# Performance work log

Measured on AMD Instinct MI355X. Metric: run time of the kernel, lower is better.

## Reference

```python
import jax, jax.numpy as jnp
import numpy as np
import math

BS, H, L, D = 4, 8, 1024, 64
P = 513  # max_path_num + 1


def setup_inputs() -> dict:
    key = jax.random.key(0)
    ks = jax.random.split(key, 6)
    return {
        "query": jax.random.normal(ks[0], (BS, H, L, D), dtype=jnp.float32),
        "key": jax.random.normal(ks[1], (BS, H, L, D), dtype=jnp.float32),
        "value": jax.random.normal(ks[2], (BS, H, L, D), dtype=jnp.float32),
        "relation": jax.random.normal(ks[3], (BS, P, D), dtype=jnp.float32),
        "path_map": jax.random.randint(ks[4], (BS, L, L), 0, P, dtype=jnp.int32),
        "mask": jax.random.randint(ks[5], (BS, 1, L, L), 0, 2, dtype=jnp.int32),
    }


def reference(query, key, value, relation, path_map, mask):
    bs, h, Lc, d = query.shape
    p = relation.shape[1]
    # content score: bs,h,L,L
    score = jnp.einsum("bhik,bhjk->bhij", query, key)
    # relation score. Torch gathers with index of shape (bs,1,L,L) from a
    # (bs,h,L,P) tensor, which reads head 0 only and broadcasts over heads.
    score_r_h0 = jnp.einsum("bik,bpk->bip", query[:, 0], relation)  # bs,L,P
    gathered = jnp.take_along_axis(score_r_h0, path_map, axis=-1)   # bs,L,L
    score = score + gathered[:, None, :, :]
    scores = score / math.sqrt(d)
    scores = jnp.where(mask == 0, jnp.float32(-1e9), scores)
    p_attn = jax.nn.softmax(scores, axis=-1)  # bs,h,L,L
    attn_sum = jnp.einsum("bhij,bhjk->bhik", p_attn, value)
    # scatter-add attention probs into relation buckets: bs,h,L,P
    b_ix = jnp.arange(bs)[:, None, None, None]
    h_ix = jnp.arange(h)[None, :, None, None]
    i_ix = jnp.arange(Lc)[None, None, :, None]
    pm = jnp.broadcast_to(path_map[:, None, :, :], (bs, h, Lc, Lc))
    r_buckets = jnp.zeros((bs, h, Lc, p), dtype=p_attn.dtype).at[b_ix, h_ix, i_ix, pm].add(p_attn)
    r_attn_sum = jnp.einsum("bhip,bpk->bhik", r_buckets, relation)
    attn_sum = attn_sum + r_attn_sum
    return (attn_sum, p_attn)
```

## Files before the change

kernel.cpp:

```cpp
#include <hip/hip_runtime.h>


#define BSZ 4
#define NH 8
#define LSEQ 1024
#define DH 64
#define NP 513
#define TI 16
#define NT 1024
#define SRX 548
#define RTC 544

#define NQE (BSZ*NH*LSEQ*DH)
#define NRT (BSZ*DH*RTC)
#define NSR (BSZ*LSEQ*NP)
#define NGPW (2*BSZ*LSEQ*LSEQ)
#define OFF_QH 0
#define OFF_QL (NQE)
#define OFF_KH (2*NQE)
#define OFF_KL (3*NQE)
#define OFF_VT (4*NQE)
#define OFF_RT (5*NQE)
#define OFF_SR (5*NQE + NRT)
#define OFF_GP (5*NQE + NRT + NSR)
#define WS_NEED ((size_t)(OFF_GP + NGPW) * 2)

#define NB_QK 4096
#define NB_VT 512
#define NB_RT 544
#define NB_SR 256
#define NB_P1 (NB_QK + NB_VT + NB_RT + NB_SR)

typedef __attribute__((ext_vector_type(8))) short bf16x8;
typedef __attribute__((ext_vector_type(4))) float f32x4;
typedef __attribute__((ext_vector_type(4))) ushort u16x4;
typedef __attribute__((ext_vector_type(4))) uint u32x4;

__device__ __forceinline__ ushort f2bf(float x) {
    uint u = __float_as_uint(x);
    u += 0x7FFFu + ((u >> 16) & 1u);
    return (ushort)(u >> 16);
}
__device__ __forceinline__ float bf2f(ushort h) {
    return __uint_as_float(((uint)h) << 16);
}


__global__ __launch_bounds__(256) void prep1(
    const float* __restrict__ Q, const float* __restrict__ K,
    const float* __restrict__ V, const float* __restrict__ REL,
    ushort* __restrict__ ws)
{
    __shared__ float sT[64 * 65];
    const int bid = blockIdx.x;
    const int tid = threadIdx.x;

    if (bid < NB_QK) {
        const int n4 = NQE / 4;
        int i = bid * 256 + tid;
        int isK = i >= n4;
        int base = i - isK * n4;
        float4 v = ((const float4*)(isK ? K : Q))[base];
        float xs[4] = {v.x, v.y, v.z, v.w};
        u16x4 hh, ll;
        #pragma unroll
        for (int e = 0; e < 4; ++e) {
            ushort hi = f2bf(xs[e]);
            hh[e] = hi;
            ll[e] = f2bf(xs[e] - bf2f(hi));
        }
        *(u16x4*)(ws + (isK ? OFF_KH : OFF_QH) + (size_t)base * 4) = hh;
        *(u16x4*)(ws + (isK ? OFF_KL : OFF_QL) + (size_t)base * 4) = ll;
    } else if (bid < NB_QK + NB_VT) {
        const int vb = bid - NB_QK;
        const int bh = vb >> 4;
        const int j0 = (vb & 15) * 64;
        const float* Vb = V + ((size_t)bh << 16);
        for (int i = tid; i < 1024; i += 256) {
            int jr = i >> 4, c4 = i & 15;
            float4 vv = *(const float4*)(Vb + (size_t)(j0 + jr) * DH + c4 * 4);
            float* dst = &sT[jr * 65 + c4 * 4];
            dst[0] = vv.x; dst[1] = vv.y; dst[2] = vv.z; dst[3] = vv.w;
        }
        __syncthreads();
        const int d = tid >> 2, jseg = tid & 3;
        ushort* dst = ws + OFF_VT + ((size_t)bh << 16) + (size_t)d * LSEQ + j0 + jseg * 16;
        #pragma unroll
        for (int g = 0; g < 4; ++g) {
            u16x4 o;
            #pragma unroll
            for (int e = 0; e < 4; ++e)
                o[e] = f2bf(sT[(jseg * 16 + g * 4 + e) * 65 + d]);
            *(u16x4*)(dst + g * 4) = o;
        }
    } else if (bid < NB_QK + NB_VT + NB_RT) {
        int i = (bid - NB_QK - NB_VT) * 256 + tid;
        int b = i / (DH * RTC);
        int r = i - b * (DH * RTC);
        int d = r / RTC;
        int p = r - d * RTC;
        float x = (p < NP) ? REL[((size_t)b * NP + p) * DH + d] : 0.f;
        ws[OFF_RT + i] = f2bf(x);
    } else {
        const int sb = bid - (NB_QK + NB_VT + NB_RT);
        const int it = sb & 63, b = sb >> 6;
        const int i0 = it * TI;
        const int w = tid >> 6, l = tid & 63, lg = l >> 4, lm = l & 15;

        const float* Qb0 = Q + ((size_t)b * NH) * LSEQ * DH;
        const float* RELb = REL + (size_t)b * NP * DH;
        ushort* SRb = ws + OFF_SR + (size_t)b * LSEQ * NP;

        bf16x8 qh[2], ql[2];
        #pragma unroll
        for (int ks = 0; ks < 2; ++ks) {
            const float* qs = Qb0 + (size_t)(i0 + lm) * DH + ks * 32 + lg * 8;
            float4 v0 = *(const float4*)(qs);
            float4 v1 = *(const float4*)(qs + 4);
            float xs[8] = {v0.x, v0.y, v0.z, v0.w, v1.x, v1.y, v1.z, v1.w};
            #pragma unroll
            for (int e = 0; e < 8; ++e) {
                ushort hi = f2bf(xs[e]);
                qh[ks][e] = (short)hi;
                ql[ks][e] = (short)f2bf(xs[e] - bf2f(hi));
            }
        }

        for (int ct = w; ct < 33; ct += 4) {
            int p0 = ct * 16;
            int prow = p0 + lm; if (prow > 512) prow = 512;
            f32x4 a0 = {0.f, 0.f, 0.f, 0.f};
            #pragma unroll
            for (int ks = 0; ks < 2; ++ks) {
                const float* bsrc = RELb + (size_t)prow * DH + ks * 32 + lg * 8;
                float4 v0 = *(const float4*)(bsrc);
                float4 v1 = *(const float4*)(bsrc + 4);
                float xs[8] = {v0.x, v0.y, v0.z, v0.w, v1.x, v1.y, v1.z, v1.w};
                bf16x8 bh8, bl8;
                #pragma unroll
                for (int e = 0; e < 8; ++e) {
                    ushort hi = f2bf(xs[e]);
                    bh8[e] = (short)hi;
                    bl8[e] = (short)f2bf(xs[e] - bf2f(hi));
                }
                a0 = __builtin_amdgcn_mfma_f32_16x16x32_bf16(qh[ks], bh8, a0, 0, 0, 0);
                a0 = __builtin_amdgcn_mfma_f32_16x16x32_bf16(ql[ks], bh8, a0, 0, 0, 0);
                a0 = __builtin_amdgcn_mfma_f32_16x16x32_bf16(qh[ks], bl8, a0, 0, 0, 0);
            }
            if (p0 + lm < NP) {
                #pragma unroll
                for (int e = 0; e < 4; ++e)
                    SRb[(size_t)(i0 + 4 * lg + e) * NP + p0 + lm] = f2bf(a0[e]);
            }
        }
    }
}


__global__ __launch_bounds__(256) void prep2(
    const int* __restrict__ PM, const int* __restrict__ MASK,
    ushort* __restrict__ ws)
{
    __shared__ ushort sSR[4 * 520];
    const int tid = threadIdx.x;
    const int bid = blockIdx.x;
    const int b = bid >> 8;
    const int row0 = (bid & 255) * 4;

    const ushort* SRb = ws + OFF_SR + (size_t)b * LSEQ * NP;
    uint* GPb = (uint*)(ws + OFF_GP) + (size_t)b * LSEQ * LSEQ;
    const int* PMb = PM + (size_t)b * LSEQ * LSEQ;
    const int* MKb = MASK + (size_t)b * LSEQ * LSEQ;

    for (int i = tid; i < 4 * 520; i += 256) {
        int row = i / 520, col = i - row * 520;
        if (col < NP) sSR[row * 520 + col] = SRb[(size_t)(row0 + row) * NP + col];
    }
    __syncthreads();

    #pragma unroll
    for (int r = 0; r < 4; ++r) {
        int idx4 = r * 256 + tid;
        int row = idx4 >> 8;
        int c0 = (idx4 & 255) * 4;
        size_t off = (size_t)(row0 + row) * LSEQ + c0;
        int4 pm4 = *(const int4*)(PMb + off);
        int4 mk4 = *(const int4*)(MKb + off);
        const ushort* srow = &sSR[row * 520];
        u32x4 o;
        o[0] = ((uint)(mk4.x ? srow[pm4.x] : 0xFF62u) << 16) | (uint)pm4.x;
        o[1] = ((uint)(mk4.y ? srow[pm4.y] : 0xFF62u) << 16) | (uint)pm4.y;
        o[2] = ((uint)(mk4.z ? srow[pm4.z] : 0xFF62u) << 16) | (uint)pm4.z;
        o[3] = ((uint)(mk4.w ? srow[pm4.w] : 0xFF62u) << 16) | (uint)pm4.w;
        *(u32x4*)(GPb + off) = o;
    }
}


__global__ __launch_bounds__(NT, 4) void raa_main(
    const ushort* __restrict__ ws,
    float* __restrict__ OUT_A, float* __restrict__ OUT_P)
{
    __shared__ float  X[TI * SRX];
    __shared__ ushort sPb[TI * 1024];
    __shared__ float  sAttn[TI * DH];
    __shared__ float  sRedM[16 * 17];
    __shared__ float  sRedS[16 * 17];

    const int tid = threadIdx.x;
    const int w  = tid >> 6;
    const int l  = tid & 63;
    const int lg = l >> 4;
    const int lm = l & 15;

    const int it = blockIdx.x, h = blockIdx.y, b = blockIdx.z;
    const int i0 = it * TI;
    const int bh = b * NH + h;

    const ushort* Qh = ws + OFF_QH + (size_t)bh * LSEQ * DH;
    const ushort* Ql = ws + OFF_QL + (size_t)bh * LSEQ * DH;
    const ushort* Kh = ws + OFF_KH + (size_t)bh * LSEQ * DH;
    const ushort* Kl = ws + OFF_KL + (size_t)bh * LSEQ * DH;
    const ushort* Vt = ws + OFF_VT + (size_t)bh * DH * LSEQ;
    const ushort* Rt = ws + OFF_RT + (size_t)b * DH * RTC;
    const uint*   GPb = (const uint*)(ws + OFF_GP) + (size_t)b * LSEQ * LSEQ;

    #pragma unroll
    for (int z = 0; z < 9; ++z) {
        int idx = z * NT + tid;
        if (idx < TI * SRX) X[idx] = 0.f;
    }
    sAttn[tid] = 0.f;

    uint gp[16];
    #pragma unroll
    for (int t = 0; t < 4; ++t) {
        #pragma unroll
        for (int e = 0; e < 4; ++e) {
            int col = (4 * w + t) * 16 + lm;
            int row = 4 * lg + e;
            gp[t * 4 + e] = GPb[(size_t)(i0 + row) * LSEQ + col];
        }
    }

    bf16x8 qhh[2], qhl[2];
    #pragma unroll
    for (int ks = 0; ks < 2; ++ks) {
        size_t ao = (size_t)(i0 + lm) * DH + ks * 32 + lg * 8;
        qhh[ks] = *(const bf16x8*)(Qh + ao);
        qhl[ks] = *(const bf16x8*)(Ql + ao);
    }

    f32x4 acc[4];
    bf16x8 kh_c[2], kl_c[2], kh_n[2], kl_n[2];
    {
        size_t bo = (size_t)(4 * w * 16 + lm) * DH + lg * 8;
        kh_c[0] = *(const bf16x8*)(Kh + bo);      kl_c[0] = *(const bf16x8*)(Kl + bo);
        kh_c[1] = *(const bf16x8*)(Kh + bo + 32); kl_c[1] = *(const bf16x8*)(Kl + bo + 32);
    }
    #pragma unroll
    for (int t = 0; t < 4; ++t) {
        if (t < 3) {
            size_t bo = (size_t)((4 * w + t + 1) * 16 + lm) * DH + lg * 8;
            kh_n[0] = *(const bf16x8*)(Kh + bo);      kl_n[0] = *(const bf16x8*)(Kl + bo);
            kh_n[1] = *(const bf16x8*)(Kh + bo + 32); kl_n[1] = *(const bf16x8*)(Kl + bo + 32);
        }
        acc[t] = (f32x4){0.f, 0.f, 0.f, 0.f};
        #pragma unroll
        for (int ks = 0; ks < 2; ++ks) {
            acc[t] = __builtin_amdgcn_mfma_f32_16x16x32_bf16(qhh[ks], kh_c[ks], acc[t], 0, 0, 0);
            acc[t] = __builtin_amdgcn_mfma_f32_16x16x32_bf16(qhl[ks], kh_c[ks], acc[t], 0, 0, 0);
            acc[t] = __builtin_amdgcn_mfma_f32_16x16x32_bf16(qhh[ks], kl_c[ks], acc[t], 0, 0, 0);
        }
        #pragma unroll
        for (int ks = 0; ks < 2; ++ks) {
            kh_c[ks] = kh_n[ks]; kl_c[ks] = kl_n[ks];
        }
    }

    #pragma unroll
    for (int i = 0; i < 16; ++i) {
        int t = i >> 2, e = i & 3;
        float g = bf2f((ushort)(gp[i] >> 16));
        acc[t][e] = (g < -1e30f) ? -1e9f : (acc[t][e] + g) * 0.125f;
    }

    float mw[4], c4v[4];
    #pragma unroll
    for (int e = 0; e < 4; ++e) {
        float m = fmaxf(fmaxf(acc[0][e], acc[1][e]), fmaxf(acc[2][e], acc[3][e]));
        #pragma unroll
        for (int o = 8; o >= 1; o >>= 1) m = fmaxf(m, __shfl_xor(m, o));
        mw[e] = m;
        float s = 0.f;
        #pragma unroll
        for (int t = 0; t < 4; ++t) {
            float v = __expf(acc[t][e] - m);
            acc[t][e] = v;
            s += v;
        }
        #pragma unroll
        for (int o = 8; o >= 1; o >>= 1) s += __shfl_xor(s, o);
        if (lm == 0) {
            sRedM[(4 * lg + e) * 17 + w] = m;
            sRedS[(4 * lg + e) * 17 + w] = s;
        }
    }
    __syncthreads();
    #pragma unroll
    for (int e = 0; e < 4; ++e) {
        int row = 4 * lg + e;
        float mv = sRedM[row * 17 + lm];
        float sv = sRedS[row * 17 + lm];
        float m = mv;
        #pragma unroll
        for (int o = 8; o >= 1; o >>= 1) m = fmaxf(m, __shfl_xor(m, o));
        float sp = sv * __expf(mv - m);
        #pragma unroll
        for (int o = 8; o >= 1; o >>= 1) sp += __shfl_xor(sp, o);
        c4v[e] = __expf(mw[e] - m) / sp;
    }

    #pragma unroll
    for (int t = 0; t < 4; ++t) {
        int col = (4 * w + t) * 16 + lm;
        #pragma unroll
        for (int e = 0; e < 4; ++e) {
            int row = 4 * lg + e;
            float p = acc[t][e] * c4v[e];
            sPb[row * 1024 + (((col >> 3) ^ (row & 7)) << 3) + (col & 7)] = f2bf(p);
            atomicAdd(&X[row * SRX + (int)(gp[t * 4 + e] & 0xFFFFu)], p);
        }
    }
    __syncthreads();

    const size_t pbase = ((size_t)bh * LSEQ + i0) * LSEQ;
    #pragma unroll
    for (int g = 0; g < 4; ++g) {
        int elem = g * 4096 + tid * 4;
        int r = elem >> 10, cc = elem & 1023;
        int ad = r * 1024 + (((cc >> 3) ^ (r & 7)) << 3) + (cc & 7);
        u16x4 pv = *(const u16x4*)&sPb[ad];
        float4 o4 = make_float4(bf2f(pv[0]), bf2f(pv[1]), bf2f(pv[2]), bf2f(pv[3]));
        *(float4*)(OUT_P + pbase + (size_t)r * LSEQ + cc) = o4;
    }

    if (w < 8) {
        int ct = w >> 1, jh = w & 1;
        int d0 = ct * 16;
        f32x4 pa = {0.f, 0.f, 0.f, 0.f};
        #pragma unroll 4
        for (int ks = 0; ks < 16; ++ks) {
            int j0 = jh * 512 + ks * 32;
            int ch = (j0 >> 3) + lg;
            bf16x8 a = *(const bf16x8*)&sPb[lm * 1024 + ((ch ^ (lm & 7)) << 3)];
            bf16x8 bb = *(const bf16x8*)(Vt + (size_t)(d0 + lm) * LSEQ + j0 + lg * 8);
            pa = __builtin_amdgcn_mfma_f32_16x16x32_bf16(a, bb, pa, 0, 0, 0);
        }
        #pragma unroll
        for (int e = 0; e < 4; ++e)
            atomicAdd(&sAttn[(4 * lg + e) * DH + d0 + lm], pa[e]);
    } else {
        int ct = (w - 8) >> 1, ph = w & 1;
        int d0 = ct * 16;
        int nks = ph ? 8 : 9;
        int pb0 = ph ? 288 : 0;
        f32x4 pa = {0.f, 0.f, 0.f, 0.f};
        for (int ks = 0; ks < nks; ++ks) {
            int p0 = pb0 + ks * 32;
            float x8[8];
            *(float4*)&x8[0] = *(const float4*)&X[lm * SRX + p0 + lg * 8];
            *(float4*)&x8[4] = *(const float4*)&X[lm * SRX + p0 + lg * 8 + 4];
            bf16x8 a;
            #pragma unroll
            for (int e = 0; e < 8; ++e)
                a[e] = (short)f2bf(x8[e]);
            bf16x8 bb = *(const bf16x8*)(Rt + (size_t)(d0 + lm) * RTC + p0 + lg * 8);
            pa = __builtin_amdgcn_mfma_f32_16x16x32_bf16(a, bb, pa, 0, 0, 0);
        }
        #pragma unroll
        for (int e = 0; e < 4; ++e)
            atomicAdd(&sAttn[(4 * lg + e) * DH + d0 + lm], pa[e]);
    }
    __syncthreads();

    OUT_A[((size_t)bh * LSEQ + i0 + (tid >> 6)) * DH + (tid & 63)] = sAttn[tid];
}


__global__ __launch_bounds__(NT, 4) void raa_fallback(
    const float* __restrict__ Q, const float* __restrict__ K,
    const float* __restrict__ V, const float* __restrict__ REL,
    const int* __restrict__ PM, const int* __restrict__ MASK,
    float* __restrict__ OUT_A, float* __restrict__ OUT_P)
{
    __shared__ ushort sQh[TI * 64];
    __shared__ ushort sQl[TI * 64];
    __shared__ float  sR[TI * NP];
    __shared__ ushort sPb[TI * 1024];
    __shared__ float  sAttn[TI * 64];
    __shared__ float  sRed[16 * 17];
    __shared__ float  sFin[16];

    const int tid = threadIdx.x;
    const int w  = tid >> 6;
    const int l  = tid & 63;
    const int lg = l >> 4;
    const int lm = l & 15;

    const int it = blockIdx.x, h = blockIdx.y, b = blockIdx.z;
    const int i0 = it * TI;

    const float* Qb0  = Q + ((size_t)b * NH + 0) * LSEQ * DH;
    const float* Qbh  = Q + ((size_t)b * NH + h) * LSEQ * DH;
    const float* Kbh  = K + ((size_t)b * NH + h) * LSEQ * DH;
    const float* Vbh  = V + ((size_t)b * NH + h) * LSEQ * DH;
    const float* RELb = REL + (size_t)b * NP * DH;
    const int*   PMb  = PM  + (size_t)b * LSEQ * LSEQ;
    const int*   MKb  = MASK + (size_t)b * LSEQ * LSEQ;

    {
        int row = tid >> 6, kk = tid & 63;
        float x = Qb0[(size_t)(i0 + row) * DH + kk];
        ushort hi = f2bf(x);
        ushort lo = f2bf(x - bf2f(hi));
        int ad = row * 64 + (((kk >> 3) ^ (row & 7)) << 3) + (kk & 7);
        sQh[ad] = hi; sQl[ad] = lo;
        sAttn[tid] = 0.f;
    }
    __syncthreads();

    bf16x8 qh[2], ql[2];
    #pragma unroll
    for (int ks = 0; ks < 2; ++ks) {
        int ch = lg + 4 * ks;
        int ad = lm * 64 + ((ch ^ (lm & 7)) << 3);
        qh[ks] = *(const bf16x8*)&sQh[ad];
        ql[ks] = *(const bf16x8*)&sQl[ad];
    }
    __syncthreads();

    {
        int row = tid >> 6, kk = tid & 63;
        float x = Qbh[(size_t)(i0 + row) * DH + kk];
        ushort hi = f2bf(x);
        ushort lo = f2bf(x - bf2f(hi));
        int ad = row * 64 + (((kk >> 3) ^ (row & 7)) << 3) + (kk & 7);
        sQh[ad] = hi; sQl[ad] = lo;
    }

    for (int ct = w; ct < 33; ct += 16) {
        int p0 = ct * 16;
        int prow = p0 + lm; if (prow > 512) prow = 512;
        const float* bsrc = RELb + (size_t)prow * DH + 8 * lg;
        f32x4 acc = {0.f, 0.f, 0.f, 0.f};
        #pragma unroll
        for (int ks = 0; ks < 2; ++ks) {
            float4 v0 = *(const float4*)(bsrc + ks * 32);
            float4 v1 = *(const float4*)(bsrc + ks * 32 + 4);
            float xs[8] = {v0.x, v0.y, v0.z, v0.w, v1.x, v1.y, v1.z, v1.w};
            bf16x8 bh, bl;
            #pragma unroll
            for (int e = 0; e < 8; ++e) {
                ushort hi = f2bf(xs[e]);
                bh[e] = (short)hi;
                bl[e] = (short)f2bf(xs[e] - bf2f(hi));
            }
            acc = __builtin_amdgcn_mfma_f32_16x16x32_bf16(qh[ks], bh, acc, 0, 0, 0);
            acc = __builtin_amdgcn_mfma_f32_16x16x32_bf16(ql[ks], bh, acc, 0, 0, 0);
            acc = __builtin_amdgcn_mfma_f32_16x16x32_bf16(qh[ks], bl, acc, 0, 0, 0);
        }
        int pcol = p0 + lm;
        if (pcol < NP) {
            #pragma unroll
            for (int e = 0; e < 4; ++e)
                sR[(4 * lg + e) * NP + pcol] = acc[e];
        }
    }
    __syncthreads();

    #pragma unroll
    for (int ks = 0; ks < 2; ++ks) {
        int ch = lg + 4 * ks;
        int ad = lm * 64 + ((ch ^ (lm & 7)) << 3);
        qh[ks] = *(const bf16x8*)&sQh[ad];
        ql[ks] = *(const bf16x8*)&sQl[ad];
    }
    f32x4 acc[4];
    #pragma unroll
    for (int t = 0; t < 4; ++t) {
        int j = (4 * w + t) * 16 + lm;
        const float* bsrc = Kbh + (size_t)j * DH + 8 * lg;
        acc[t] = (f32x4){0.f, 0.f, 0.f, 0.f};
        #pragma unroll
        for (int ks = 0; ks < 2; ++ks) {
            float4 v0 = *(const float4*)(bsrc + ks * 32);
            float4 v1 = *(const float4*)(bsrc + ks * 32 + 4);
            float xs[8] = {v0.x, v0.y, v0.z, v0.w, v1.x, v1.y, v1.z, v1.w};
            bf16x8 bh, bl;
            #pragma unroll
            for (int e = 0; e < 8; ++e) {
                ushort hi = f2bf(xs[e]);
                bh[e] = (short)hi;
                bl[e] = (short)f2bf(xs[e] - bf2f(hi));
            }
            acc[t] = __builtin_amdgcn_mfma_f32_16x16x32_bf16(qh[ks], bh, acc[t], 0, 0, 0);
            acc[t] = __builtin_amdgcn_mfma_f32_16x16x32_bf16(ql[ks], bh, acc[t], 0, 0, 0);
            acc[t] = __builtin_amdgcn_mfma_f32_16x16x32_bf16(qh[ks], bl, acc[t], 0, 0, 0);
        }
    }

    #pragma unroll
    for (int t = 0; t < 4; ++t) {
        int col = (4 * w + t) * 16 + lm;
        #pragma unroll
        for (int e = 0; e < 4; ++e) {
            int row = 4 * lg + e;
            size_t off = (size_t)(i0 + row) * LSEQ + col;
            int pm = PMb[off];
            int mk = MKb[off];
            float g = sR[row * NP + pm];
            acc[t][e] = (mk == 0) ? -1e9f : (acc[t][e] + g) * 0.125f;
        }
    }
    __syncthreads();
    for (int idx = tid; idx < TI * NP; idx += NT) sR[idx] = 0.f;
    __syncthreads();

    float Mr[4];
    #pragma unroll
    for (int e = 0; e < 4; ++e) {
        float m = fmaxf(fmaxf(acc[0][e], acc[1][e]), fmaxf(acc[2][e], acc[3][e]));
        #pragma unroll
        for (int o = 8; o >= 1; o >>= 1) m = fmaxf(m, __shfl_xor(m, o));
        Mr[e] = m;
    }
    if (lm == 0) {
        #pragma unroll
        for (int e = 0; e < 4; ++e) sRed[(4 * lg + e) * 17 + w] = Mr[e];
    }
    __syncthreads();
    if (w == 0 && l < 16) {
        float m = -INFINITY;
        for (int ww = 0; ww < 16; ++ww) m = fmaxf(m, sRed[l * 17 + ww]);
        sFin[l] = m;
    }
    __syncthreads();
    #pragma unroll
    for (int e = 0; e < 4; ++e) Mr[e] = sFin[4 * lg + e];

    float Sr[4];
    #pragma unroll
    for (int e = 0; e < 4; ++e) {
        float s = 0.f;
        #pragma unroll
        for (int t = 0; t < 4; ++t) {
            float v = __expf(acc[t][e] - Mr[e]);
            acc[t][e] = v;
            s += v;
        }
        #pragma unroll
        for (int o = 8; o >= 1; o >>= 1) s += __shfl_xor(s, o);
        Sr[e] = s;
    }
    if (lm == 0) {
        #pragma unroll
        for (int e = 0; e < 4; ++e) sRed[(4 * lg + e) * 17 + w] = Sr[e];
    }
    __syncthreads();
    if (w == 0 && l < 16) {
        float s = 0.f;
        for (int ww = 0; ww < 16; ++ww) s += sRed[l * 17 + ww];
        sFin[l] = s;
    }
    __syncthreads();

    float inv[4];
    #pragma unroll
    for (int e = 0; e < 4; ++e) inv[e] = 1.0f / sFin[4 * lg + e];

    const size_t pbase = (((size_t)b * NH + h) * LSEQ + i0) * LSEQ;
    #pragma unroll
    for (int t = 0; t < 4; ++t) {
        int col = (4 * w + t) * 16 + lm;
        #pragma unroll
        for (int e = 0; e < 4; ++e) {
            int row = 4 * lg + e;
            float p = acc[t][e] * inv[e];
            OUT_P[pbase + (size_t)row * LSEQ + col] = p;
            int ad = row * 1024 + (((col >> 3) ^ (row & 7)) << 3) + (col & 7);
            sPb[ad] = f2bf(p);
            int pm = PMb[(size_t)(i0 + row) * LSEQ + col];
            atomicAdd(&sR[row * NP + pm], p);
        }
    }
    __syncthreads();

    if (w < 8) {
        int ct = w >> 1, jh = w & 1;
        int d = ct * 16 + lm;
        f32x4 pa = {0.f, 0.f, 0.f, 0.f};
        for (int ks = 0; ks < 16; ++ks) {
            int j0 = jh * 512 + ks * 32;
            int ch = (j0 >> 3) + lg;
            bf16x8 a = *(const bf16x8*)&sPb[lm * 1024 + ((ch ^ (lm & 7)) << 3)];
            const float* vs = Vbh + (size_t)(j0 + 8 * lg) * DH + d;
            bf16x8 bb;
            #pragma unroll
            for (int e = 0; e < 8; ++e) bb[e] = (short)f2bf(vs[(size_t)e * DH]);
            pa = __builtin_amdgcn_mfma_f32_16x16x32_bf16(a, bb, pa, 0, 0, 0);
        }
        #pragma unroll
        for (int e = 0; e < 4; ++e)
            atomicAdd(&sAttn[(4 * lg + e) * 64 + d], pa[e]);
    } else {
        int ct = (w - 8) >> 1, ph = w & 1;
        int d = ct * 16 + lm;
        int nks = ph ? 9 : 8;
        f32x4 pa = {0.f, 0.f, 0.f, 0.f};
        for (int ks = 0; ks < nks; ++ks) {
            int p0 = ph * 256 + ks * 32 + 8 * lg;
            bf16x8 a, bb;
            #pragma unroll
            for (int e = 0; e < 8; ++e) {
                int pp = p0 + e;
                float av = (pp < NP) ? sR[lm * NP + pp] : 0.f;
                a[e] = (short)f2bf(av);
                int pc = (pp < NP) ? pp : (NP - 1);
                bb[e] = (short)f2bf(RELb[(size_t)pc * DH + d]);
            }
            pa = __builtin_amdgcn_mfma_f32_16x16x32_bf16(a, bb, pa, 0, 0, 0);
        }
        #pragma unroll
        for (int e = 0; e < 4; ++e)
            atomicAdd(&sAttn[(4 * lg + e) * 64 + d], pa[e]);
    }
    __syncthreads();

    {
        int row = tid >> 6, col = tid & 63;
        OUT_A[(((size_t)b * NH + h) * LSEQ + i0 + row) * DH + col] =
            sAttn[row * 64 + col];
    }
}

extern "C" void kernel_launch(void* const* d_in, const int* in_sizes, int n_in,
                              void* d_out, int out_size, void* d_ws, size_t ws_size,
                              hipStream_t stream) {
    const float* q    = (const float*)d_in[0];
    const float* k    = (const float*)d_in[1];
    const float* v    = (const float*)d_in[2];
    const float* rel  = (const float*)d_in[3];
    const int*   pm   = (const int*)d_in[4];
    const int*   mask = (const int*)d_in[5];
    float* out_a = (float*)d_out;
    float* out_p = (float*)d_out + (size_t)BSZ * NH * LSEQ * DH;

    dim3 grid(LSEQ / TI, NH, BSZ);
    if (ws_size >= WS_NEED && d_ws != nullptr) {
        ushort* ws = (ushort*)d_ws;
        prep1<<<NB_P1, 256, 0, stream>>>(q, k, v, rel, ws);
        prep2<<<1024, 256, 0, stream>>>(pm, mask, ws);
        raa_main<<<grid, NT, 0, stream>>>((const ushort*)ws, out_a, out_p);
    } else {
        raa_fallback<<<grid, NT, 0, stream>>>(q, k, v, rel, pm, mask, out_a, out_p);
    }
}
```

Measured before the change: 555.6 us.

## Split fused attention kernel into QK-softmax and PV/relation kernels with XCD-aware mapping

Splits the single 1024-thread main kernel into two 512-thread kernels. The first computes scores and softmax and writes fp32 probabilities straight to the output. The second re-reads those probabilities from global memory to do the scatter-add into relation buckets and both PV matmuls. Block indices are remapped so blocks sharing a batch-head land on the same XCD, and prep1 now puts the relation-score blocks first, split into two halves. This is meant to cut LDS pressure and raise occupancy, at the cost of re-reading the 128MB probability tensor from global memory and an extra launch.

```diff
diff --git a/kernel.cpp b/kernel.cpp
--- a/kernel.cpp
+++ b/kernel.cpp
@@ -7,7 +7,6 @@
 #define DH 64
 #define NP 513
 #define TI 16
-#define NT 1024
 #define SRX 548
 #define RTC 544
 
@@ -25,11 +24,11 @@
 #define OFF_GP (5*NQE + NRT + NSR)
 #define WS_NEED ((size_t)(OFF_GP + NGPW) * 2)
 
+#define NB_SR 512
 #define NB_QK 4096
 #define NB_VT 512
 #define NB_RT 544
-#define NB_SR 256
-#define NB_P1 (NB_QK + NB_VT + NB_RT + NB_SR)
+#define NB_P1 (NB_SR + NB_QK + NB_VT + NB_RT)
 
 typedef __attribute__((ext_vector_type(8))) short bf16x8;
 typedef __attribute__((ext_vector_type(4))) float f32x4;
@@ -55,55 +54,10 @@
     const int bid = blockIdx.x;
     const int tid = threadIdx.x;
 
-    if (bid < NB_QK) {
-        const int n4 = NQE / 4;
-        int i = bid * 256 + tid;
-        int isK = i >= n4;
-        int base = i - isK * n4;
-        float4 v = ((const float4*)(isK ? K : Q))[base];
-        float xs[4] = {v.x, v.y, v.z, v.w};
-        u16x4 hh, ll;
-        #pragma unroll
-        for (int e = 0; e < 4; ++e) {
-            ushort hi = f2bf(xs[e]);
-            hh[e] = hi;
-            ll[e] = f2bf(xs[e] - bf2f(hi));
-        }
-        *(u16x4*)(ws + (isK ? OFF_KH : OFF_QH) + (size_t)base * 4) = hh;
-        *(u16x4*)(ws + (isK ? OFF_KL : OFF_QL) + (size_t)base * 4) = ll;
-    } else if (bid < NB_QK + NB_VT) {
-        const int vb = bid - NB_QK;
-        const int bh = vb >> 4;
-        const int j0 = (vb & 15) * 64;
-        const float* Vb = V + ((size_t)bh << 16);
-        for (int i = tid; i < 1024; i += 256) {
-            int jr = i >> 4, c4 = i & 15;
-            float4 vv = *(const float4*)(Vb + (size_t)(j0 + jr) * DH + c4 * 4);
-            float* dst = &sT[jr * 65 + c4 * 4];
-            dst[0] = vv.x; dst[1] = vv.y; dst[2] = vv.z; dst[3] = vv.w;
-        }
-        __syncthreads();
-        const int d = tid >> 2, jseg = tid & 3;
-        ushort* dst = ws + OFF_VT + ((size_t)bh << 16) + (size_t)d * LSEQ + j0 + jseg * 16;
-        #pragma unroll
-        for (int g = 0; g < 4; ++g) {
-            u16x4 o;
-            #pragma unroll
-            for (int e = 0; e < 4; ++e)
-                o[e] = f2bf(sT[(jseg * 16 + g * 4 + e) * 65 + d]);
-            *(u16x4*)(dst + g * 4) = o;
-        }
-    } else if (bid < NB_QK + NB_VT + NB_RT) {
-        int i = (bid - NB_QK - NB_VT) * 256 + tid;
-        int b = i / (DH * RTC);
-        int r = i - b * (DH * RTC);
-        int d = r / RTC;
-        int p = r - d * RTC;
-        float x = (p < NP) ? REL[((size_t)b * NP + p) * DH + d] : 0.f;
-        ws[OFF_RT + i] = f2bf(x);
-    } else {
-        const int sb = bid - (NB_QK + NB_VT + NB_RT);
-        const int it = sb & 63, b = sb >> 6;
+    if (bid < NB_SR) {
+        const int b = bid >> 7;
+        const int r = bid & 127;
+        const int it = r >> 1, half = r & 1;
         const int i0 = it * TI;
         const int w = tid >> 6, l = tid & 63, lg = l >> 4, lm = l & 15;
 
@@ -126,7 +80,8 @@
             }
         }
 
-        for (int ct = w; ct < 33; ct += 4) {
+        int ctb = half ? 33 : 16;
+        for (int ct = half * 16 + w; ct < ctb; ct += 4) {
             int p0 = ct * 16;
             int prow = p0 + lm; if (prow > 512) prow = 512;
             f32x4 a0 = {0.f, 0.f, 0.f, 0.f};
@@ -153,6 +108,52 @@
                     SRb[(size_t)(i0 + 4 * lg + e) * NP + p0 + lm] = f2bf(a0[e]);
             }
         }
+    } else if (bid < NB_SR + NB_QK) {
+        const int n4 = NQE / 4;
+        int i = (bid - NB_SR) * 256 + tid;
+        int isK = i >= n4;
+        int base = i - isK * n4;
+        float4 v = ((const float4*)(isK ? K : Q))[base];
+        float xs[4] = {v.x, v.y, v.z, v.w};
+        u16x4 hh, ll;
+        #pragma unroll
+        for (int e = 0; e < 4; ++e) {
+            ushort hi = f2bf(xs[e]);
+            hh[e] = hi;
+            ll[e] = f2bf(xs[e] - bf2f(hi));
+        }
+        *(u16x4*)(ws + (isK ? OFF_KH : OFF_QH) + (size_t)base * 4) = hh;
+        *(u16x4*)(ws + (isK ? OFF_KL : OFF_QL) + (size_t)base * 4) = ll;
+    } else if (bid < NB_SR + NB_QK + NB_VT) {
+        const int vb = bid - (NB_SR + NB_QK);
+        const int bh = vb >> 4;
+        const int j0 = (vb & 15) * 64;
+        const float* Vb = V + ((size_t)bh << 16);
+        for (int i = tid; i < 1024; i += 256) {
+            int jr = i >> 4, c4 = i & 15;
+            float4 vv = *(const float4*)(Vb + (size_t)(j0 + jr) * DH + c4 * 4);
+            float* dst = &sT[jr * 65 + c4 * 4];
+            dst[0] = vv.x; dst[1] = vv.y; dst[2] = vv.z; dst[3] = vv.w;
+        }
+        __syncthreads();
+        const int d = tid >> 2, jseg = tid & 3;
+        ushort* dst = ws + OFF_VT + ((size_t)bh << 16) + (size_t)d * LSEQ + j0 + jseg * 16;
+        #pragma unroll
+        for (int g = 0; g < 4; ++g) {
+            u16x4 o;
+            #pragma unroll
+            for (int e = 0; e < 4; ++e)
+                o[e] = f2bf(sT[(jseg * 16 + g * 4 + e) * 65 + d]);
+            *(u16x4*)(dst + g * 4) = o;
+        }
+    } else {
+        int i = (bid - (NB_SR + NB_QK + NB_VT)) * 256 + tid;
+        int b = i / (DH * RTC);
+        int r = i - b * (DH * RTC);
+        int d = r / RTC;
+        int p = r - d * RTC;
+        float x = (p < NP) ? REL[((size_t)b * NP + p) * DH + d] : 0.f;
+        ws[OFF_RT + i] = f2bf(x);
     }
 }
 
@@ -197,15 +198,11 @@
 }
 
 
-__global__ __launch_bounds__(NT, 4) void raa_main(
-    const ushort* __restrict__ ws,
-    float* __restrict__ OUT_A, float* __restrict__ OUT_P)
+__global__ __launch_bounds__(512, 4) void raa_qks(
+    const ushort* __restrict__ ws, float* __restrict__ OUT_P)
 {
-    __shared__ float  X[TI * SRX];
-    __shared__ ushort sPb[TI * 1024];
-    __shared__ float  sAttn[TI * DH];
-    __shared__ float  sRedM[16 * 17];
-    __shared__ float  sRedS[16 * 17];
+    __shared__ float sRedM[16 * 9];
+    __shared__ float sRedS[16 * 9];
 
     const int tid = threadIdx.x;
     const int w  = tid >> 6;
@@ -213,33 +210,29 @@
     const int lg = l >> 4;
     const int lm = l & 15;
 
-    const int it = blockIdx.x, h = blockIdx.y, b = blockIdx.z;
-    const int i0 = it * TI;
-    const int bh = b * NH + h;
+    const int bid = blockIdx.x;
+    const int xcd = bid & 7;
+    const int idx = bid >> 3;
+    const int bh  = (xcd << 2) + (idx >> 6);
+    const int it  = idx & 63;
+    const int b   = bh >> 3;
+    const int i0  = it * TI;
 
     const ushort* Qh = ws + OFF_QH + (size_t)bh * LSEQ * DH;
     const ushort* Ql = ws + OFF_QL + (size_t)bh * LSEQ * DH;
     const ushort* Kh = ws + OFF_KH + (size_t)bh * LSEQ * DH;
     const ushort* Kl = ws + OFF_KL + (size_t)bh * LSEQ * DH;
-    const ushort* Vt = ws + OFF_VT + (size_t)bh * DH * LSEQ;
-    const ushort* Rt = ws + OFF_RT + (size_t)b * DH * RTC;
     const uint*   GPb = (const uint*)(ws + OFF_GP) + (size_t)b * LSEQ * LSEQ;
 
-    #pragma unroll
-    for (int z = 0; z < 9; ++z) {
-        int idx = z * NT + tid;
-        if (idx < TI * SRX) X[idx] = 0.f;
-    }
-    sAttn[tid] = 0.f;
-
-    uint gp[16];
-    #pragma unroll
-    for (int t = 0; t < 4; ++t) {
+    float gf[32];
+    #pragma unroll
+    for (int t = 0; t < 8; ++t) {
         #pragma unroll
         for (int e = 0; e < 4; ++e) {
-            int col = (4 * w + t) * 16 + lm;
+            int col = (8 * w + t) * 16 + lm;
             int row = 4 * lg + e;
-            gp[t * 4 + e] = GPb[(size_t)(i0 + row) * LSEQ + col];
+            uint g = GPb[(size_t)(i0 + row) * LSEQ + col];
+            gf[t * 4 + e] = bf2f((ushort)(g >> 16));
         }
     }
 
@@ -251,50 +244,43 @@
         qhl[ks] = *(const bf16x8*)(Ql + ao);
     }
 
-    f32x4 acc[4];
-    bf16x8 kh_c[2], kl_c[2], kh_n[2], kl_n[2];
-    {
-        size_t bo = (size_t)(4 * w * 16 + lm) * DH + lg * 8;
-        kh_c[0] = *(const bf16x8*)(Kh + bo);      kl_c[0] = *(const bf16x8*)(Kl + bo);
-        kh_c[1] = *(const bf16x8*)(Kh + bo + 32); kl_c[1] = *(const bf16x8*)(Kl + bo + 32);
-    }
-    #pragma unroll
-    for (int t = 0; t < 4; ++t) {
-        if (t < 3) {
-            size_t bo = (size_t)((4 * w + t + 1) * 16 + lm) * DH + lg * 8;
-            kh_n[0] = *(const bf16x8*)(Kh + bo);      kl_n[0] = *(const bf16x8*)(Kl + bo);
-            kh_n[1] = *(const bf16x8*)(Kh + bo + 32); kl_n[1] = *(const bf16x8*)(Kl + bo + 32);
-        }
-        acc[t] = (f32x4){0.f, 0.f, 0.f, 0.f};
-        #pragma unroll
-        for (int ks = 0; ks < 2; ++ks) {
-            acc[t] = __builtin_amdgcn_mfma_f32_16x16x32_bf16(qhh[ks], kh_c[ks], acc[t], 0, 0, 0);
-            acc[t] = __builtin_amdgcn_mfma_f32_16x16x32_bf16(qhl[ks], kh_c[ks], acc[t], 0, 0, 0);
-            acc[t] = __builtin_amdgcn_mfma_f32_16x16x32_bf16(qhh[ks], kl_c[ks], acc[t], 0, 0, 0);
-        }
-        #pragma unroll
-        for (int ks = 0; ks < 2; ++ks) {
-            kh_c[ks] = kh_n[ks]; kl_c[ks] = kl_n[ks];
-        }
-    }
-
-    #pragma unroll
-    for (int i = 0; i < 16; ++i) {
+    f32x4 acc[8];
+    #pragma unroll
+    for (int t = 0; t < 8; ++t) {
+        size_t bo = (size_t)((8 * w + t) * 16 + lm) * DH + lg * 8;
+        bf16x8 kh0 = *(const bf16x8*)(Kh + bo);
+        bf16x8 kl0 = *(const bf16x8*)(Kl + bo);
+        bf16x8 kh1 = *(const bf16x8*)(Kh + bo + 32);
+        bf16x8 kl1 = *(const bf16x8*)(Kl + bo + 32);
+        f32x4 a = {0.f, 0.f, 0.f, 0.f};
+        a = __builtin_amdgcn_mfma_f32_16x16x32_bf16(qhh[0], kh0, a, 0, 0, 0);
+        a = __builtin_amdgcn_mfma_f32_16x16x32_bf16(qhl[0], kh0, a, 0, 0, 0);
+        a = __builtin_amdgcn_mfma_f32_16x16x32_bf16(qhh[0], kl0, a, 0, 0, 0);
+        a = __builtin_amdgcn_mfma_f32_16x16x32_bf16(qhh[1], kh1, a, 0, 0, 0);
+        a = __builtin_amdgcn_mfma_f32_16x16x32_bf16(qhl[1], kh1, a, 0, 0, 0);
+        a = __builtin_amdgcn_mfma_f32_16x16x32_bf16(qhh[1], kl1, a, 0, 0, 0);
+        acc[t] = a;
+    }
+
+    #pragma unroll
+    for (int i = 0; i < 32; ++i) {
         int t = i >> 2, e = i & 3;
-        float g = bf2f((ushort)(gp[i] >> 16));
+        float g = gf[i];
         acc[t][e] = (g < -1e30f) ? -1e9f : (acc[t][e] + g) * 0.125f;
     }
 
     float mw[4], c4v[4];
     #pragma unroll
     for (int e = 0; e < 4; ++e) {
-        float m = fmaxf(fmaxf(acc[0][e], acc[1][e]), fmaxf(acc[2][e], acc[3][e]));
+        float m = acc[0][e];
+        #pragma unroll
+        for (int t = 1; t < 8; ++t) m = fmaxf(m, acc[t][e]);
         #pragma unroll
         for (int o = 8; o >= 1; o >>= 1) m = fmaxf(m, __shfl_xor(m, o));
         mw[e] = m;
         float s = 0.f;
         #pragma unroll
-        for (int t = 0; t < 4; ++t) {
+        for (int t = 0; t < 8; ++t) {
             float v = __expf(acc[t][e] - m);
             acc[t][e] = v;
             s += v;
@@ -302,93 +288,135 @@
         #pragma unroll
         for (int o = 8; o >= 1; o >>= 1) s += __shfl_xor(s, o);
         if (lm == 0) {
-            sRedM[(4 * lg + e) * 17 + w] = m;
-            sRedS[(4 * lg + e) * 17 + w] = s;
+            sRedM[(4 * lg + e) * 9 + w] = m;
+            sRedS[(4 * lg + e) * 9 + w] = s;
         }
     }
     __syncthreads();
     #pragma unroll
     for (int e = 0; e < 4; ++e) {
         int row = 4 * lg + e;
-        float mv = sRedM[row * 17 + lm];
-        float sv = sRedS[row * 17 + lm];
+        float mv = sRedM[row * 9 + (lm & 7)];
+        float sv = sRedS[row * 9 + (lm & 7)];
         float m = mv;
         #pragma unroll
-        for (int o = 8; o >= 1; o >>= 1) m = fmaxf(m, __shfl_xor(m, o));
+        for (int o = 4; o >= 1; o >>= 1) m = fmaxf(m, __shfl_xor(m, o));
         float sp = sv * __expf(mv - m);
         #pragma unroll
-        for (int o = 8; o >= 1; o >>= 1) sp += __shfl_xor(sp, o);
+        for (int o = 4; o >= 1; o >>= 1) sp += __shfl_xor(sp, o);
         c4v[e] = __expf(mw[e] - m) / sp;
     }
 
-    #pragma unroll
-    for (int t = 0; t < 4; ++t) {
-        int col = (4 * w + t) * 16 + lm;
+    const size_t pbase = ((size_t)bh * LSEQ + i0) * LSEQ;
+    #pragma unroll
+    for (int t = 0; t < 8; ++t) {
+        int col = (8 * w + t) * 16 + lm;
         #pragma unroll
         for (int e = 0; e < 4; ++e) {
             int row = 4 * lg + e;
-            float p = acc[t][e] * c4v[e];
-            sPb[row * 1024 + (((col >> 3) ^ (row & 7)) << 3) + (col & 7)] = f2bf(p);
-            atomicAdd(&X[row * SRX + (int)(gp[t * 4 + e] & 0xFFFFu)], p);
-        }
-    }
-    __syncthreads();
-
-    const size_t pbase = ((size_t)bh * LSEQ + i0) * LSEQ;
-    #pragma unroll
-    for (int g = 0; g < 4; ++g) {
-        int elem = g * 4096 + tid * 4;
-        int r = elem >> 10, cc = elem & 1023;
-        int ad = r * 1024 + (((cc >> 3) ^ (r & 7)) << 3) + (cc & 7);
-        u16x4 pv = *(const u16x4*)&sPb[ad];
-        float4 o4 = make_float4(bf2f(pv[0]), bf2f(pv[1]), bf2f(pv[2]), bf2f(pv[3]));
-        *(float4*)(OUT_P + pbase + (size_t)r * LSEQ + cc) = o4;
-    }
-
-    if (w < 8) {
-        int ct = w >> 1, jh = w & 1;
-        int d0 = ct * 16;
-        f32x4 pa = {0.f, 0.f, 0.f, 0.f};
+            OUT_P[pbase + (size_t)row * LSEQ + col] = acc[t][e] * c4v[e];
+        }
+    }
+}
+
+
+__global__ __launch_bounds__(512, 4) void raa_pv(
+    const ushort* __restrict__ ws, const float* __restrict__ P_in,
+    float* __restrict__ OUT_A)
+{
+    __shared__ float X[TI * SRX];
+    __shared__ float sAttn[TI * DH];
+
+    const int tid = threadIdx.x;
+    const int w  = tid >> 6;
+    const int l  = tid & 63;
+    const int lg = l >> 4;
+    const int lm = l & 15;
+
+    const int bid = blockIdx.x;
+    const int xcd = bid & 7;
+    const int idx = bid >> 3;
+    const int bh  = (xcd << 2) + (idx >> 6);
+    const int it  = idx & 63;
+    const int b   = bh >> 3;
+    const int i0  = it * TI;
+
+    const ushort* Vt = ws + OFF_VT + (size_t)bh * DH * LSEQ;
+    const ushort* Rt = ws + OFF_RT + (size_t)b * DH * RTC;
+    const uint*   GPb = (const uint*)(ws + OFF_GP) + (size_t)b * LSEQ * LSEQ;
+    const float*  Pb = P_in + ((size_t)bh * LSEQ + i0) * LSEQ;
+
+    for (int z = tid; z < TI * SRX; z += 512) X[z] = 0.f;
+    for (int z = tid; z < TI * DH; z += 512) sAttn[z] = 0.f;
+    __syncthreads();
+
+    {
+        int row = 2 * w + (l >> 5);
+        int l32 = l & 31;
+        const float* prow = Pb + (size_t)row * LSEQ;
+        const uint*  grow = GPb + (size_t)(i0 + row) * LSEQ;
+        float* xrow = &X[row * SRX];
+        #pragma unroll
+        for (int itr = 0; itr < 8; ++itr) {
+            int c0 = itr * 128 + l32 * 4;
+            float4 p4 = *(const float4*)(prow + c0);
+            u32x4 g4 = *(const u32x4*)(grow + c0);
+            atomicAdd(&xrow[g4[0] & 0xFFFFu], p4.x);
+            atomicAdd(&xrow[g4[1] & 0xFFFFu], p4.y);
+            atomicAdd(&xrow[g4[2] & 0xFFFFu], p4.z);
+            atomicAdd(&xrow[g4[3] & 0xFFFFu], p4.w);
+        }
+    }
+    __syncthreads();
+
+    const int d0 = (w & 3) * 16;
+    f32x4 pa = {0.f, 0.f, 0.f, 0.f};
+    if (w < 4) {
         #pragma unroll 4
-        for (int ks = 0; ks < 16; ++ks) {
-            int j0 = jh * 512 + ks * 32;
-            int ch = (j0 >> 3) + lg;
-            bf16x8 a = *(const bf16x8*)&sPb[lm * 1024 + ((ch ^ (lm & 7)) << 3)];
+        for (int ks = 0; ks < 32; ++ks) {
+            int j0 = ks * 32;
+            const float* ps = Pb + (size_t)lm * LSEQ + j0 + lg * 8;
+            float4 a0 = *(const float4*)(ps);
+            float4 a1 = *(const float4*)(ps + 4);
+            bf16x8 a;
+            a[0] = (short)f2bf(a0.x); a[1] = (short)f2bf(a0.y);
+            a[2] = (short)f2bf(a0.z); a[3] = (short)f2bf(a0.w);
+            a[4] = (short)f2bf(a1.x); a[5] = (short)f2bf(a1.y);
+            a[6] = (short)f2bf(a1.z); a[7] = (short)f2bf(a1.w);
             bf16x8 bb = *(const bf16x8*)(Vt + (size_t)(d0 + lm) * LSEQ + j0 + lg * 8);
             pa = __builtin_amdgcn_mfma_f32_16x16x32_bf16(a, bb, pa, 0, 0, 0);
         }
-        #pragma unroll
-        for (int e = 0; e < 4; ++e)
-            atomicAdd(&sAttn[(4 * lg + e) * DH + d0 + lm], pa[e]);
     } else {
-        int ct = (w - 8) >> 1, ph = w & 1;
-        int d0 = ct * 16;
-        int nks = ph ? 8 : 9;
-        int pb0 = ph ? 288 : 0;
-        f32x4 pa = {0.f, 0.f, 0.f, 0.f};
-        for (int ks = 0; ks < nks; ++ks) {
-            int p0 = pb0 + ks * 32;
-            float x8[8];
-            *(float4*)&x8[0] = *(const float4*)&X[lm * SRX + p0 + lg * 8];
-            *(float4*)&x8[4] = *(const float4*)&X[lm * SRX + p0 + lg * 8 + 4];
+        #pragma unroll 4
+        for (int ks = 0; ks < 17; ++ks) {
+            int p0 = ks * 32;
+            const float* xs = &X[lm * SRX + p0 + lg * 8];
+            float4 a0 = *(const float4*)(xs);
+            float4 a1 = *(const float4*)(xs + 4);
             bf16x8 a;
-            #pragma unroll
-            for (int e = 0; e < 8; ++e)
-                a[e] = (short)f2bf(x8[e]);
+            a[0] = (short)f2bf(a0.x); a[1] = (short)f2bf(a0.y);
+            a[2] = (short)f2bf(a0.z); a[3] = (short)f2bf(a0.w);
+            a[4] = (short)f2bf(a1.x); a[5] = (short)f2bf(a1.y);
+            a[6] = (short)f2bf(a1.z); a[7] = (short)f2bf(a1.w);
             bf16x8 bb = *(const bf16x8*)(Rt + (size_t)(d0 + lm) * RTC + p0 + lg * 8);
             pa = __builtin_amdgcn_mfma_f32_16x16x32_bf16(a, bb, pa, 0, 0, 0);
         }
-        #pragma unroll
-        for (int e = 0; e < 4; ++e)
-            atomicAdd(&sAttn[(4 * lg + e) * DH + d0 + lm], pa[e]);
-    }
-    __syncthreads();
-
-    OUT_A[((size_t)bh * LSEQ + i0 + (tid >> 6)) * DH + (tid & 63)] = sAttn[tid];
-}
-
-
-__global__ __launch_bounds__(NT, 4) void raa_fallback(
+    }
+    #pragma unroll
+    for (int e = 0; e < 4; ++e)
+        atomicAdd(&sAttn[(4 * lg + e) * DH + d0 + lm], pa[e]);
+    __syncthreads();
+
+    {
+        int row = tid >> 5;
+        int c0 = (tid & 31) * 2;
+        *(float2*)(OUT_A + ((size_t)bh * LSEQ + i0 + row) * DH + c0) =
+            *(const float2*)&sAttn[row * DH + c0];
+    }
+}
+
+
+__global__ __launch_bounds__(1024, 4) void raa_fallback(
     const float* __restrict__ Q, const float* __restrict__ K,
     const float* __restrict__ V, const float* __restrict__ REL,
     const int* __restrict__ PM, const int* __restrict__ MASK,
@@ -524,7 +552,7 @@
         }
     }
     __syncthreads();
-    for (int idx = tid; idx < TI * NP; idx += NT) sR[idx] = 0.f;
+    for (int idxx = tid; idxx < TI * NP; idxx += 1024) sR[idxx] = 0.f;
     __syncthreads();
 
     float Mr[4];
@@ -656,13 +684,14 @@
     float* out_a = (float*)d_out;
     float* out_p = (float*)d_out + (size_t)BSZ * NH * LSEQ * DH;
 
-    dim3 grid(LSEQ / TI, NH, BSZ);
     if (ws_size >= WS_NEED && d_ws != nullptr) {
         ushort* ws = (ushort*)d_ws;
         prep1<<<NB_P1, 256, 0, stream>>>(q, k, v, rel, ws);
         prep2<<<1024, 256, 0, stream>>>(pm, mask, ws);
-        raa_main<<<grid, NT, 0, stream>>>((const ushort*)ws, out_a, out_p);
+        raa_qks<<<2048, 512, 0, stream>>>((const ushort*)ws, out_p);
+        raa_pv<<<2048, 512, 0, stream>>>((const ushort*)ws, out_p, out_a);
     } else {
-        raa_fallback<<<grid, NT, 0, stream>>>(q, k, v, rel, pm, mask, out_a, out_p);
-    }
-}
+        dim3 grid(LSEQ / TI, NH, BSZ);
+        raa_fallback<<<grid, 1024, 0, stream>>>(q, k, v, rel, pm, mask, out_a, out_p);
+    }
+}
```

Result: faster. 474.1 us (-14.7%).
